# Kernel optimization log

Hardware: AMD Instinct MI355X
Metric: run time of the kernel (lower is better)

The kernel has to match this reference:

```python
import jax, jax.numpy as jnp
from jax import lax
import numpy as np

DEPTH_MIN, DEPTH_MAX = 0.0, 100.0
VOL_D, VOL_H, VOL_W = 128, 128, 128


def setup_inputs() -> dict:
    key = jax.random.key(0)
    k1, k2 = jax.random.split(key)
    # depth values span the full depth_range so all D slices get hit
    depth_map = jax.random.uniform(k1, (8, 1, 512, 512), dtype=jnp.float32) * 100.0
    x_ray = jax.random.uniform(k2, (8, 1, 512, 512), dtype=jnp.float32)
    return {"depth_map": depth_map, "x_ray": x_ray}


def reference(depth_map, x_ray):
    B = depth_map.shape[0]
    D, H, W = VOL_D, VOL_H, VOL_W

    # F.interpolate(..., mode='bilinear', align_corners=False) == jax.image.resize bilinear
    resize = lambda x: jax.image.resize(x, (B, 1, H, W), method='bilinear')
    depth_r = resize(depth_map)   # [B,1,H,W]
    xray_r = resize(x_ray)        # [B,1,H,W]

    nd = (depth_r - DEPTH_MIN) / (DEPTH_MAX - DEPTH_MIN)
    d_idx = jnp.clip((nd * (D - 1)).astype(jnp.int32), 0, D - 1)  # [B,1,H,W]

    # 5-tap gaussian splat along depth (vectorized scatter-add over all b,h,w,offset)
    offsets = jnp.arange(-2, 3)                                   # [5]
    weights = jnp.exp(-0.5 * (offsets.astype(jnp.float32) ** 2))  # [5]
    targets = d_idx[..., None] + offsets                          # [B,1,H,W,5]
    valid = (targets >= 0) & (targets < D)
    targets_c = jnp.clip(targets, 0, D - 1)
    vals = xray_r[..., None] * weights * valid.astype(jnp.float32)  # [B,1,H,W,5]

    bb = jnp.arange(B)[:, None, None, None, None]
    hh = jnp.arange(H)[None, None, :, None, None]
    ww = jnp.arange(W)[None, None, None, :, None]
    # volume stored depth-last for the scatter, then transposed to [B,1,D,H,W]
    vol = jnp.zeros((B, 1, H, W, D), jnp.float32).at[bb, 0, hh, ww, targets_c].add(vals)
    vol = jnp.transpose(vol, (0, 1, 4, 2, 3))  # [B,1,D,H,W]

    # avg_pool3d(kernel=3, stride=1, pad=1), count_include_pad=True -> divide by 27
    summed = lax.reduce_window(vol, 0.0, lax.add,
                               (1, 1, 3, 3, 3), (1, 1, 1, 1, 1),
                               [(0, 0), (0, 0), (1, 1), (1, 1), (1, 1)])
    return summed / 27.0
```

## Files before the change

### kernel.cpp

```cpp
#include <hip/hip_runtime.h>

#define NB 8
#define IN_HW 512
#define OHW 128
#define VOLD 128

#define E1f 0.60653065971263342f
#define E2f 0.13533528323661270f

#define CSTR 132

__global__ __launch_bounds__(256) void resize_kernel(
    const float* __restrict__ depth, const float* __restrict__ xray,
    int* __restrict__ didx, float* __restrict__ xr)
{
    int idx = blockIdx.x * blockDim.x + threadIdx.x;
    int j = idx & (OHW - 1);
    int i = (idx >> 7) & (OHW - 1);
    int b = idx >> 14;

    const double rawd[8] = {0.125, 0.375, 0.625, 0.875, 0.875, 0.625, 0.375, 0.125};

    int r0 = 4 * i - 2, c0 = 4 * j - 2;
    double wr[8], wc[8];
    double sr = 0.0, sc = 0.0;
#pragma unroll
    for (int k = 0; k < 8; ++k) {
        int r = r0 + k;
        wr[k] = (r >= 0 && r < IN_HW) ? rawd[k] : 0.0; sr += wr[k];
        int c = c0 + k;
        wc[k] = (c >= 0 && c < IN_HW) ? rawd[k] : 0.0; sc += wc[k];
    }
    double invd = 1.0 / (sr * sc);
    float  invf = (float)invd;

    int f0 = j - 1; if (f0 < 0) f0 = 0;
    int f2 = j + 1; if (f2 > (IN_HW / 4) - 1) f2 = (IN_HW / 4) - 1;
    int f1 = j;

    const float4* dbase = (const float4*)(depth + (size_t)b * IN_HW * IN_HW);
    const float4* xbase = (const float4*)(xray  + (size_t)b * IN_HW * IN_HW);

    double accD = 0.0;
    float  accX = 0.f;
#pragma unroll
    for (int k = 0; k < 8; ++k) {
        if (wr[k] == 0.0) continue;
        int r = r0 + k;
        const float4* drow = dbase + (size_t)r * (IN_HW / 4);
        const float4* xrow = xbase + (size_t)r * (IN_HW / 4);
        float4 d0 = drow[f0], d1 = drow[f1], d2 = drow[f2];
        float4 x0 = xrow[f0], x1 = xrow[f1], x2 = xrow[f2];
        float dt[8] = {d0.z, d0.w, d1.x, d1.y, d1.z, d1.w, d2.x, d2.y};
        float xt[8] = {x0.z, x0.w, x1.x, x1.y, x1.z, x1.w, x2.x, x2.y};
        double rd = 0.0;
        float  rx = 0.f;
#pragma unroll
        for (int l = 0; l < 8; ++l) {
            rd += wc[l] * (double)dt[l];
            rx += (float)wc[l] * xt[l];
        }
        accD += wr[k] * rd;
        accX += (float)wr[k] * rx;
    }
    accD *= invd;
    accX *= invf;

    double nd = accD * (1.0 / 100.0);
    int di = (int)(nd * 127.0);
    di = min(max(di, 0), VOLD - 1);

    didx[idx] = di;
    xr[idx]   = accX;
}

__global__ __launch_bounds__(256) void splat_pool_kernel(
    const int* __restrict__ didx, const float* __restrict__ xr,
    float* __restrict__ out)
{
    __shared__ __align__(16) float col[130][CSTR];

    int t   = threadIdx.x;
    int blk = blockIdx.x;
    int h = blk & (OHW - 1);
    int b = blk >> 7;

    float xv[3]; int dv[3];
    if (t < 130) {
        int wc = t - 1;
#pragma unroll
        for (int r = 0; r < 3; ++r) {
            int hr = h + r - 1;
            xv[r] = 0.f; dv[r] = 1 << 20;
            if (hr >= 0 && hr < OHW && wc >= 0 && wc < OHW) {
                int g = (b * OHW + hr) * OHW + wc;
                xv[r] = xr[g]; dv[r] = didx[g];
            }
        }
    }

    {
        float4* colv = (float4*)&col[0][0];
        for (int k = t; k < (130 * CSTR) / 4; k += 256)
            colv[k] = float4{0.f, 0.f, 0.f, 0.f};
    }
    __syncthreads();

    if (t < 130) {
        const float S[7] = {E2f, E2f + E1f, E2f + E1f + 1.f, 1.f + 2.f * E1f,
                            1.f + E1f + E2f, E1f + E2f, E2f};
        const float A[7] = {E2f, E2f + E1f, E1f + 1.f, 1.f + E1f,
                            E1f + E2f, E2f, 0.f};
        const float Z[7] = {0.f, E2f, E2f + E1f, 1.f + E1f,
                            1.f + E1f, E1f + E2f, E2f};
#pragma unroll 1
        for (int r = 0; r < 3; ++r) {
            float x = xv[r];
            int  di = dv[r];
#pragma unroll
            for (int o = -3; o <= 3; ++o) {
                int d = di + o;
                if (d < 0 || d > VOLD - 1) continue;
                float w = S[o + 3];
                if (d == 0)            w = A[o + 3];
                else if (d == VOLD-1)  w = Z[o + 3];
                col[t][d] += x * w;
            }
        }
    }
    __syncthreads();

    int w    = t & (OHW - 1);
    int half = t >> 7;
    const float inv27 = 1.f / 27.f;
    const float4* colv = (const float4*)&col[0][0];
    int base = w * (CSTR / 4) + half * 16;
    float* obase = out + ((size_t)(b * VOLD + half * 64) * OHW + h) * OHW + w;
#pragma unroll
    for (int q = 0; q < 16; ++q) {
        float4 a = colv[base + q];
        float4 c1 = colv[base + q + (CSTR / 4)];
        float4 c2 = colv[base + q + 2 * (CSTR / 4)];
        float4 v;
        v.x = (a.x + c1.x + c2.x) * inv27;
        v.y = (a.y + c1.y + c2.y) * inv27;
        v.z = (a.z + c1.z + c2.z) * inv27;
        v.w = (a.w + c1.w + c2.w) * inv27;
        float* o = obase + (size_t)(q * 4) * OHW * OHW;
        o[0 * OHW * OHW] = v.x;
        o[1 * OHW * OHW] = v.y;
        o[2 * OHW * OHW] = v.z;
        o[3 * OHW * OHW] = v.w;
    }
}

extern "C" void kernel_launch(void* const* d_in, const int* in_sizes, int n_in,
                              void* d_out, int out_size, void* d_ws, size_t ws_size,
                              hipStream_t stream)
{
    const float* depth = (const float*)d_in[0];
    const float* xray  = (const float*)d_in[1];
    float* out = (float*)d_out;

    const int NPIX = NB * OHW * OHW;
    int*   didx = (int*)d_ws;
    float* xrs  = (float*)((char*)d_ws + (size_t)NPIX * sizeof(int));

    resize_kernel<<<NPIX / 256, 256, 0, stream>>>(depth, xray, didx, xrs);
    splat_pool_kernel<<<NB * OHW, 256, 0, stream>>>(didx, xrs, out);
}
```

Measured before the change: 97.57 us.

## Fuse resize into splat-pool kernel and widen blocks to 512 threads

Merges the bilinear resize kernel into the splat/pool kernel, so each block recomputes the three resized rows it needs straight from the input images instead of reading a workspace buffer. The block size doubles to 512 threads so the three rows are splatted in parallel with shared-memory atomics, and the output store loop is split across four thread groups. This removes one launch and the intermediate global round trip, at the cost of computing each resized pixel three times and adding LDS atomic contention.

Result: slower. 106.9 us (+9.5%).

```diff
diff --git a/kernel.cpp b/kernel.cpp
--- a/kernel.cpp
+++ b/kernel.cpp
@@ -10,72 +10,8 @@
 
 #define CSTR 132
 
-__global__ __launch_bounds__(256) void resize_kernel(
+__global__ __launch_bounds__(512, 2) void fused_kernel(
     const float* __restrict__ depth, const float* __restrict__ xray,
-    int* __restrict__ didx, float* __restrict__ xr)
-{
-    int idx = blockIdx.x * blockDim.x + threadIdx.x;
-    int j = idx & (OHW - 1);
-    int i = (idx >> 7) & (OHW - 1);
-    int b = idx >> 14;
-
-    const double rawd[8] = {0.125, 0.375, 0.625, 0.875, 0.875, 0.625, 0.375, 0.125};
-
-    int r0 = 4 * i - 2, c0 = 4 * j - 2;
-    double wr[8], wc[8];
-    double sr = 0.0, sc = 0.0;
-#pragma unroll
-    for (int k = 0; k < 8; ++k) {
-        int r = r0 + k;
-        wr[k] = (r >= 0 && r < IN_HW) ? rawd[k] : 0.0; sr += wr[k];
-        int c = c0 + k;
-        wc[k] = (c >= 0 && c < IN_HW) ? rawd[k] : 0.0; sc += wc[k];
-    }
-    double invd = 1.0 / (sr * sc);
-    float  invf = (float)invd;
-
-    int f0 = j - 1; if (f0 < 0) f0 = 0;
-    int f2 = j + 1; if (f2 > (IN_HW / 4) - 1) f2 = (IN_HW / 4) - 1;
-    int f1 = j;
-
-    const float4* dbase = (const float4*)(depth + (size_t)b * IN_HW * IN_HW);
-    const float4* xbase = (const float4*)(xray  + (size_t)b * IN_HW * IN_HW);
-
-    double accD = 0.0;
-    float  accX = 0.f;
-#pragma unroll
-    for (int k = 0; k < 8; ++k) {
-        if (wr[k] == 0.0) continue;
-        int r = r0 + k;
-        const float4* drow = dbase + (size_t)r * (IN_HW / 4);
-        const float4* xrow = xbase + (size_t)r * (IN_HW / 4);
-        float4 d0 = drow[f0], d1 = drow[f1], d2 = drow[f2];
-        float4 x0 = xrow[f0], x1 = xrow[f1], x2 = xrow[f2];
-        float dt[8] = {d0.z, d0.w, d1.x, d1.y, d1.z, d1.w, d2.x, d2.y};
-        float xt[8] = {x0.z, x0.w, x1.x, x1.y, x1.z, x1.w, x2.x, x2.y};
-        double rd = 0.0;
-        float  rx = 0.f;
-#pragma unroll
-        for (int l = 0; l < 8; ++l) {
-            rd += wc[l] * (double)dt[l];
-            rx += (float)wc[l] * xt[l];
-        }
-        accD += wr[k] * rd;
-        accX += (float)wr[k] * rx;
-    }
-    accD *= invd;
-    accX *= invf;
-
-    double nd = accD * (1.0 / 100.0);
-    int di = (int)(nd * 127.0);
-    di = min(max(di, 0), VOLD - 1);
-
-    didx[idx] = di;
-    xr[idx]   = accX;
-}
-
-__global__ __launch_bounds__(256) void splat_pool_kernel(
-    const int* __restrict__ didx, const float* __restrict__ xr,
     float* __restrict__ out)
 {
     __shared__ __align__(16) float col[130][CSTR];
@@ -85,60 +21,101 @@
     int h = blk & (OHW - 1);
     int b = blk >> 7;
 
-    float xv[3]; int dv[3];
-    if (t < 130) {
-        int wc = t - 1;
+    int wc = t & (OHW - 1);
+    int r  = t >> 7;
+    int hr = h + r - 1;
+
+    float accXf = 0.f;
+    int   di    = -1000;
+
+    if (r < 3 && hr >= 0 && hr < OHW) {
+        int r0 = 4 * hr - 2, c0 = 4 * wc - 2;
+        double sr = (hr == 0 || hr == OHW - 1) ? 3.5 : 4.0;
+        double sc = (wc == 0 || wc == OHW - 1) ? 3.5 : 4.0;
+        double invd = 1.0 / (sr * sc);
+        float  invf = (float)invd;
+
+        int f0 = wc - 1; if (f0 < 0) f0 = 0;
+        int f2 = wc + 1; if (f2 > (IN_HW / 4) - 1) f2 = (IN_HW / 4) - 1;
+        int f1 = wc;
+
+        const float4* dbase = (const float4*)(depth + (size_t)b * IN_HW * IN_HW);
+        const float4* xbase = (const float4*)(xray  + (size_t)b * IN_HW * IN_HW);
+
+        bool ledge = (wc == 0);
+        bool redge = (wc == OHW - 1);
+
+        double accD = 0.0;
+        float  accX = 0.f;
 #pragma unroll
-        for (int r = 0; r < 3; ++r) {
-            int hr = h + r - 1;
-            xv[r] = 0.f; dv[r] = 1 << 20;
-            if (hr >= 0 && hr < OHW && wc >= 0 && wc < OHW) {
-                int g = (b * OHW + hr) * OHW + wc;
-                xv[r] = xr[g]; dv[r] = didx[g];
-            }
+        for (int k = 0; k < 8; ++k) {
+            int rr = r0 + k;
+            if (rr < 0 || rr >= IN_HW) continue;
+            const float4* drow = dbase + (size_t)rr * (IN_HW / 4);
+            const float4* xrow = xbase + (size_t)rr * (IN_HW / 4);
+            float4 d0 = drow[f0], d1 = drow[f1], d2 = drow[f2];
+            float4 x0 = xrow[f0], x1 = xrow[f1], x2 = xrow[f2];
+            float dt[8] = {d0.z, d0.w, d1.x, d1.y, d1.z, d1.w, d2.x, d2.y};
+            float xt[8] = {x0.z, x0.w, x1.x, x1.y, x1.z, x1.w, x2.x, x2.y};
+            if (ledge) { dt[0] = dt[1] = 0.f; xt[0] = xt[1] = 0.f; }
+            if (redge) { dt[6] = dt[7] = 0.f; xt[6] = xt[7] = 0.f; }
+            double rd = 0.125 * (double)dt[0] + 0.375 * (double)dt[1]
+                      + 0.625 * (double)dt[2] + 0.875 * (double)dt[3]
+                      + 0.875 * (double)dt[4] + 0.625 * (double)dt[5]
+                      + 0.375 * (double)dt[6] + 0.125 * (double)dt[7];
+            float  rx = 0.125f * xt[0] + 0.375f * xt[1]
+                      + 0.625f * xt[2] + 0.875f * xt[3]
+                      + 0.875f * xt[4] + 0.625f * xt[5]
+                      + 0.375f * xt[6] + 0.125f * xt[7];
+            const double rawk[8] = {0.125, 0.375, 0.625, 0.875,
+                                    0.875, 0.625, 0.375, 0.125};
+            accD += rawk[k] * rd;
+            accX += (float)rawk[k] * rx;
         }
+        accD *= invd;
+        accX *= invf;
+
+        double nd = accD * (1.0 / 100.0);
+        int dii = (int)(nd * 127.0);
+        di = min(max(dii, 0), VOLD - 1);
+        accXf = accX;
     }
 
     {
         float4* colv = (float4*)&col[0][0];
-        for (int k = t; k < (130 * CSTR) / 4; k += 256)
+        for (int k = t; k < (130 * CSTR) / 4; k += 512)
             colv[k] = float4{0.f, 0.f, 0.f, 0.f};
     }
     __syncthreads();
 
-    if (t < 130) {
+    if (di >= 0) {
         const float S[7] = {E2f, E2f + E1f, E2f + E1f + 1.f, 1.f + 2.f * E1f,
                             1.f + E1f + E2f, E1f + E2f, E2f};
         const float A[7] = {E2f, E2f + E1f, E1f + 1.f, 1.f + E1f,
                             E1f + E2f, E2f, 0.f};
         const float Z[7] = {0.f, E2f, E2f + E1f, 1.f + E1f,
                             1.f + E1f, E1f + E2f, E2f};
-#pragma unroll 1
-        for (int r = 0; r < 3; ++r) {
-            float x = xv[r];
-            int  di = dv[r];
+        float* c = &col[wc + 1][0];
 #pragma unroll
-            for (int o = -3; o <= 3; ++o) {
-                int d = di + o;
-                if (d < 0 || d > VOLD - 1) continue;
-                float w = S[o + 3];
-                if (d == 0)            w = A[o + 3];
-                else if (d == VOLD-1)  w = Z[o + 3];
-                col[t][d] += x * w;
-            }
+        for (int o = -3; o <= 3; ++o) {
+            int d = di + o;
+            if (d < 0 || d > VOLD - 1) continue;
+            float w = S[o + 3];
+            if (d == 0)            w = A[o + 3];
+            else if (d == VOLD-1)  w = Z[o + 3];
+            atomicAdd(&c[d], accXf * w);
         }
     }
     __syncthreads();
 
-    int w    = t & (OHW - 1);
-    int half = t >> 7;
+    int q4 = t >> 7;
     const float inv27 = 1.f / 27.f;
     const float4* colv = (const float4*)&col[0][0];
-    int base = w * (CSTR / 4) + half * 16;
-    float* obase = out + ((size_t)(b * VOLD + half * 64) * OHW + h) * OHW + w;
+    int base = wc * (CSTR / 4) + q4 * 8;
+    float* obase = out + ((size_t)(b * VOLD + q4 * 32) * OHW + h) * OHW + wc;
 #pragma unroll
-    for (int q = 0; q < 16; ++q) {
-        float4 a = colv[base + q];
+    for (int q = 0; q < 8; ++q) {
+        float4 a  = colv[base + q];
         float4 c1 = colv[base + q + (CSTR / 4)];
         float4 c2 = colv[base + q + 2 * (CSTR / 4)];
         float4 v;
@@ -161,11 +138,7 @@
     const float* depth = (const float*)d_in[0];
     const float* xray  = (const float*)d_in[1];
     float* out = (float*)d_out;
+    (void)d_ws; (void)ws_size;
 
-    const int NPIX = NB * OHW * OHW;
-    int*   didx = (int*)d_ws;
-    float* xrs  = (float*)((char*)d_ws + (size_t)NPIX * sizeof(int));
-
-    resize_kernel<<<NPIX / 256, 256, 0, stream>>>(depth, xray, didx, xrs);
-    splat_pool_kernel<<<NB * OHW, 256, 0, stream>>>(didx, xrs, out);
+    fused_kernel<<<NB * OHW, 512, 0, stream>>>(depth, xray, out);
 }
```

## Widen splat-pool blocks to 1024 threads with atomic LDS splatting per row

Applied to the files above, without the earlier changes.

The splat phase moves from 130 threads each looping over three input rows to 390 threads, one per (row, column), which accumulate into the shared column buffer with LDS atomic adds. The output phase spreads the 128 depth slices across 8 thread groups instead of 2, so each thread writes 16 slices rather than 64. The goal is more parallelism and shorter per-thread serial chains in both phases. In exchange it adds atomic contention on shared memory and brings 1024-thread blocks with about 68KB of LDS, which may limit how many blocks fit on a CU at once.

New measurement: 101.7 us. 1.04x slower.

```diff
diff --git a/kernel.cpp b/kernel.cpp
--- a/kernel.cpp
+++ b/kernel.cpp
@@ -74,7 +74,7 @@
     xr[idx]   = accX;
 }
 
-__global__ __launch_bounds__(256) void splat_pool_kernel(
+__global__ __launch_bounds__(1024) void splat_pool_kernel(
     const int* __restrict__ didx, const float* __restrict__ xr,
     float* __restrict__ out)
 {
@@ -85,60 +85,57 @@
     int h = blk & (OHW - 1);
     int b = blk >> 7;
 
-    float xv[3]; int dv[3];
-    if (t < 130) {
-        int wc = t - 1;
-#pragma unroll
-        for (int r = 0; r < 3; ++r) {
-            int hr = h + r - 1;
-            xv[r] = 0.f; dv[r] = 1 << 20;
-            if (hr >= 0 && hr < OHW && wc >= 0 && wc < OHW) {
-                int g = (b * OHW + hr) * OHW + wc;
-                xv[r] = xr[g]; dv[r] = didx[g];
-            }
+    float xv = 0.f;
+    int   dv = 1 << 20;
+    int   cc = 0;
+    if (t < 390) {
+        int r = t / 130;
+        cc = t - r * 130;
+        int wc = cc - 1;
+        int hr = h + r - 1;
+        if (hr >= 0 && hr < OHW && wc >= 0 && wc < OHW) {
+            int g = (b * OHW + hr) * OHW + wc;
+            xv = xr[g];
+            dv = didx[g];
         }
     }
 
     {
         float4* colv = (float4*)&col[0][0];
-        for (int k = t; k < (130 * CSTR) / 4; k += 256)
+        for (int k = t; k < (130 * CSTR) / 4; k += 1024)
             colv[k] = float4{0.f, 0.f, 0.f, 0.f};
     }
     __syncthreads();
 
-    if (t < 130) {
+    if (t < 390) {
         const float S[7] = {E2f, E2f + E1f, E2f + E1f + 1.f, 1.f + 2.f * E1f,
                             1.f + E1f + E2f, E1f + E2f, E2f};
         const float A[7] = {E2f, E2f + E1f, E1f + 1.f, 1.f + E1f,
                             E1f + E2f, E2f, 0.f};
         const float Z[7] = {0.f, E2f, E2f + E1f, 1.f + E1f,
                             1.f + E1f, E1f + E2f, E2f};
-#pragma unroll 1
-        for (int r = 0; r < 3; ++r) {
-            float x = xv[r];
-            int  di = dv[r];
+        float* c = &col[cc][0];
 #pragma unroll
-            for (int o = -3; o <= 3; ++o) {
-                int d = di + o;
-                if (d < 0 || d > VOLD - 1) continue;
-                float w = S[o + 3];
-                if (d == 0)            w = A[o + 3];
-                else if (d == VOLD-1)  w = Z[o + 3];
-                col[t][d] += x * w;
-            }
+        for (int o = -3; o <= 3; ++o) {
+            int d = dv + o;
+            if (d < 0 || d > VOLD - 1) continue;
+            float w = S[o + 3];
+            if (d == 0)            w = A[o + 3];
+            else if (d == VOLD-1)  w = Z[o + 3];
+            atomicAdd(&c[d], xv * w);
         }
     }
     __syncthreads();
 
-    int w    = t & (OHW - 1);
-    int half = t >> 7;
+    int w  = t & (OHW - 1);
+    int dq = t >> 7;
     const float inv27 = 1.f / 27.f;
     const float4* colv = (const float4*)&col[0][0];
-    int base = w * (CSTR / 4) + half * 16;
-    float* obase = out + ((size_t)(b * VOLD + half * 64) * OHW + h) * OHW + w;
+    int base = w * (CSTR / 4) + dq * 4;
+    float* obase = out + ((size_t)(b * VOLD + dq * 16) * OHW + h) * OHW + w;
 #pragma unroll
-    for (int q = 0; q < 16; ++q) {
-        float4 a = colv[base + q];
+    for (int q = 0; q < 4; ++q) {
+        float4 a  = colv[base + q];
         float4 c1 = colv[base + q + (CSTR / 4)];
         float4 c2 = colv[base + q + 2 * (CSTR / 4)];
         float4 v;
@@ -167,5 +164,5 @@
     float* xrs  = (float*)((char*)d_ws + (size_t)NPIX * sizeof(int));
 
     resize_kernel<<<NPIX / 256, 256, 0, stream>>>(depth, xray, didx, xrs);
-    splat_pool_kernel<<<NB * OHW, 256, 0, stream>>>(didx, xrs, out);
+    splat_pool_kernel<<<NB * OHW, 1024, 0, stream>>>(didx, xrs, out);
 }
```
